# Kernel tuning notes

Measured on AMD Instinct MI355X. Metric: run time of the kernel, lower is better.

The kernel has to match this reference:

```python
import jax, jax.numpy as jnp
import numpy as np

B, C, L = 8192, 1, 4096
SCALES = 5
OUT_DIM = 512
STD_FACTOR = 1.0
SQRT_HALF = 0.7071067811865476  # Haar filter coefficient 1/sqrt(2)


def setup_inputs() -> dict:
    key = jax.random.key(0)
    k1, k2 = jax.random.split(key)
    x = jax.random.normal(k1, (B, C, L), dtype=jnp.float32)
    # kaiming_uniform_(a=0): bound = sqrt(2) * sqrt(3 / fan_in)
    fan_in = L  # in_dim_wave == in_dim for dyadic Haar
    bound = np.sqrt(2.0) * np.sqrt(3.0 / fan_in)
    block_mat = jax.random.uniform(k2, (L, OUT_DIM), dtype=jnp.float32,
                                   minval=-bound, maxval=bound)
    return {"x": x, "block_mat": block_mat}


def haar_analysis(x, scales):
    """Multi-level Haar DWT over last axis. Returns [cA_n, cD_n, ..., cD_1]."""
    details = []
    cur = x
    for _ in range(scales):
        even, odd = cur[..., ::2], cur[..., 1::2]
        details.append((even - odd) * SQRT_HALF)  # highpass
        cur = (even + odd) * SQRT_HALF            # lowpass
    return [cur] + details[::-1]


def reference(x, block_mat):
    coeffs = haar_analysis(x, SCALES)
    x_freq_cat = jnp.concatenate(coeffs, axis=-1)        # [B, C, L]
    c_no = x_freq_cat.shape[-1]
    x_freq_mat = x_freq_cat.reshape(-1, c_no)            # [B*C, L]
    a = jnp.abs(x_freq_mat)
    # torch.std is unbiased (ddof=1)
    threshold = jnp.mean(a) + jnp.std(a, ddof=1) * STD_FACTOR
    mask = a > threshold
    # sparse.mm(sparse(masked x), W) == (x * mask) @ W
    x_sparse = jnp.where(mask, x_freq_mat, jnp.zeros((), x_freq_mat.dtype))
    out = jax.nn.relu(x_sparse @ block_mat)              # [B*C, OUT_DIM]
    return out.reshape(x_freq_cat.shape[:-1] + (OUT_DIM,))
```

## Files before the change

### kernel.cpp

```cpp
#include <hip/hip_runtime.h>
#include <hip/hip_bf16.h>
#include <math.h>

#define LDIM 4096
#define NROWS 8192
#define NOUT 512

static const float SQRT_HALF_F = 0.70710678118654752440f;

typedef __attribute__((ext_vector_type(8))) short short8;
typedef __attribute__((ext_vector_type(4))) float f32x4;
typedef __attribute__((ext_vector_type(8))) unsigned short u16x8;
typedef __attribute__((ext_vector_type(4))) unsigned short u16x4;
typedef __attribute__((ext_vector_type(2))) unsigned short u16x2;

#define AM_OFF   0ull
#define WT_OFF   67108864ull
#define PART_OFF (WT_OFF + 4194304ull)
#define THR_OFF  (PART_OFF + 131072ull)

__device__ inline unsigned short f2bf(float f) {
  union { float f; unsigned u; } v; v.f = f;
  unsigned r = (v.u + 0x7fffu + ((v.u >> 16) & 1u)) >> 16;
  return (unsigned short)r;
}

__device__ inline unsigned short mcvt(float f, float thr) {
  return f2bf((fabsf(f) > thr) ? f : 0.0f);
}

__device__ inline void async16(void* l, const void* g) {
  __builtin_amdgcn_global_load_lds((const __attribute__((address_space(1))) void*)g,
                                   (__attribute__((address_space(3))) void*)l, 16, 0, 0);
}

__global__ __launch_bounds__(256) void haar1_kernel(const float* __restrict__ x,
                                                    double* __restrict__ partials,
                                                    const float* __restrict__ W,
                                                    unsigned short* __restrict__ Wt) {
  if (blockIdx.x >= NROWS) {
    __shared__ float tile[32][33];
    const int wb = blockIdx.x - NROWS;
    const int bx = wb & 15;
    const int by = wb >> 4;
    const int tx = threadIdx.x & 31, ty = threadIdx.x >> 5;
#pragma unroll
    for (int j = 0; j < 4; ++j)
      tile[ty + j * 8][tx] = W[(size_t)(by * 32 + ty + j * 8) * NOUT + bx * 32 + tx];
    __syncthreads();
#pragma unroll
    for (int j = 0; j < 4; ++j)
      Wt[(size_t)(bx * 32 + ty + j * 8) * LDIM + by * 32 + tx] = f2bf(tile[tx][ty + j * 8]);
    return;
  }

  __shared__ double red[8];
  const int row = blockIdx.x;
  const int t = threadIdx.x;
  const float S = SQRT_HALF_F;

  const float4* xr = (const float4*)(x + (size_t)row * LDIM) + 4 * t;
  float v[16];
#pragma unroll
  for (int k = 0; k < 4; ++k) {
    float4 q = xr[k];
    v[4 * k] = q.x; v[4 * k + 1] = q.y; v[4 * k + 2] = q.z; v[4 * k + 3] = q.w;
  }

  double sa = 0.0, sq = 0.0;
  float a1[8], a2[4], a3[2], a4;
#pragma unroll
  for (int j = 0; j < 8; ++j) {
    float d = (v[2 * j] - v[2 * j + 1]) * S;
    a1[j] = (v[2 * j] + v[2 * j + 1]) * S;
    sa += (double)fabsf(d); sq += (double)d * (double)d;
  }
#pragma unroll
  for (int j = 0; j < 4; ++j) {
    float d = (a1[2 * j] - a1[2 * j + 1]) * S;
    a2[j] = (a1[2 * j] + a1[2 * j + 1]) * S;
    sa += (double)fabsf(d); sq += (double)d * (double)d;
  }
#pragma unroll
  for (int j = 0; j < 2; ++j) {
    float d = (a2[2 * j] - a2[2 * j + 1]) * S;
    a3[j] = (a2[2 * j] + a2[2 * j + 1]) * S;
    sa += (double)fabsf(d); sq += (double)d * (double)d;
  }
  {
    float d = (a3[0] - a3[1]) * S;
    a4 = (a3[0] + a3[1]) * S;
    sa += (double)fabsf(d); sq += (double)d * (double)d;
  }
  {
    float other = __shfl_xor(a4, 1, 64);
    if ((t & 1) == 0) {
      float d = (a4 - other) * S, ap = (a4 + other) * S;
      sa += (double)fabsf(d) + (double)fabsf(ap);
      sq += (double)d * (double)d + (double)ap * (double)ap;
    }
  }

  const int lane = t & 63, wid = t >> 6;
#pragma unroll
  for (int off = 32; off > 0; off >>= 1) {
    sa += __shfl_down(sa, off, 64);
    sq += __shfl_down(sq, off, 64);
  }
  if (lane == 0) { red[wid] = sa; red[4 + wid] = sq; }
  __syncthreads();
  if (t == 0) {
    partials[2 * (size_t)row + 0] = red[0] + red[1] + red[2] + red[3];
    partials[2 * (size_t)row + 1] = red[4] + red[5] + red[6] + red[7];
  }
}

__global__ __launch_bounds__(1024) void thr_kernel(const double* __restrict__ partials,
                                                   float* __restrict__ thr) {
  __shared__ double red[32];
  const int tid = threadIdx.x;
  double sa = 0.0, sq = 0.0;
#pragma unroll
  for (int k = 0; k < NROWS / 1024; ++k) {
    int i = tid + k * 1024;
    sa += partials[2 * i + 0];
    sq += partials[2 * i + 1];
  }
  const int lane = tid & 63, wid = tid >> 6;
#pragma unroll
  for (int off = 32; off > 0; off >>= 1) {
    sa += __shfl_down(sa, off, 64);
    sq += __shfl_down(sq, off, 64);
  }
  if (lane == 0) { red[wid] = sa; red[16 + wid] = sq; }
  __syncthreads();
  if (tid == 0) {
    double s = 0.0, q = 0.0;
#pragma unroll
    for (int i = 0; i < 16; ++i) { s += red[i]; q += red[16 + i]; }
    const double n = (double)NROWS * (double)LDIM;
    double mean = s / n;
    double var = (q - s * s / n) / (n - 1.0);
    *thr = (float)(mean + sqrt(var));
  }
}

__global__ __launch_bounds__(256) void haar2_kernel(const float* __restrict__ x,
                                                    const float* __restrict__ thrp,
                                                    unsigned short* __restrict__ Am) {
  const float thr = *thrp;
  const int row = blockIdx.x;
  const int t = threadIdx.x;
  const float S = SQRT_HALF_F;

  const float4* xr = (const float4*)(x + (size_t)row * LDIM) + 4 * t;
  float v[16];
#pragma unroll
  for (int k = 0; k < 4; ++k) {
    float4 q = xr[k];
    v[4 * k] = q.x; v[4 * k + 1] = q.y; v[4 * k + 2] = q.z; v[4 * k + 3] = q.w;
  }

  unsigned short* orow = Am + (size_t)row * LDIM;
  float a1[8], a2[4], a3[2], a4;

  u16x8 d1;
#pragma unroll
  for (int j = 0; j < 8; ++j) {
    float d = (v[2 * j] - v[2 * j + 1]) * S;
    a1[j] = (v[2 * j] + v[2 * j + 1]) * S;
    d1[j] = mcvt(d, thr);
  }
  *(u16x8*)(orow + 2048 + 8 * t) = d1;

  u16x4 d2;
#pragma unroll
  for (int j = 0; j < 4; ++j) {
    float d = (a1[2 * j] - a1[2 * j + 1]) * S;
    a2[j] = (a1[2 * j] + a1[2 * j + 1]) * S;
    d2[j] = mcvt(d, thr);
  }
  *(u16x4*)(orow + 1024 + 4 * t) = d2;

  u16x2 d3;
#pragma unroll
  for (int j = 0; j < 2; ++j) {
    float d = (a2[2 * j] - a2[2 * j + 1]) * S;
    a3[j] = (a2[2 * j] + a2[2 * j + 1]) * S;
    d3[j] = mcvt(d, thr);
  }
  *(u16x2*)(orow + 512 + 2 * t) = d3;

  {
    float d = (a3[0] - a3[1]) * S;
    a4 = (a3[0] + a3[1]) * S;
    orow[256 + t] = mcvt(d, thr);
  }
  {
    float other = __shfl_xor(a4, 1, 64);
    if ((t & 1) == 0) {
      float d = (a4 - other) * S, ap = (a4 + other) * S;
      orow[128 + t / 2] = mcvt(d, thr);
      orow[t / 2] = mcvt(ap, thr);
    }
  }
}

__global__ __launch_bounds__(512) void gemm_kernel(const unsigned short* __restrict__ Am,
                                                   const unsigned short* __restrict__ Wt,
                                                   float* __restrict__ out) {
  __shared__ __align__(16) unsigned short As[128 * 64];
  __shared__ __align__(16) unsigned short Bs[64 * 64];

  const int tid = threadIdx.x;
  const int lane = tid & 63, w = tid >> 6;
  const int quad = lane >> 4, l15 = lane & 15;
  const int wm = w >> 1, wn = w & 1;

  const int id = blockIdx.x;
  const int xcd = id & 7, slot = id >> 3;
  const int nblk = slot & 7;
  const int mblk = (slot >> 3) * 8 + xcd;
  const int n0 = nblk * 64, m0 = mblk * 128;

  f32x4 acc[2][2] = {};

  const int rl = lane >> 3;
  const int cg = (lane & 7) ^ rl;
  const unsigned short* AgBase = Am + (size_t)(m0 + rl) * LDIM + cg * 8;
  const unsigned short* BgBase = Wt + (size_t)(n0 + rl) * LDIM + cg * 8;

  for (int k0 = 0; k0 < LDIM; k0 += 64) {
#pragma unroll
    for (int j = 0; j < 2; ++j)
      async16(&As[(w * 2 + j) * 512], AgBase + (size_t)((w * 2 + j) * 8) * LDIM + k0);
    async16(&Bs[w * 512], BgBase + (size_t)(w * 8) * LDIM + k0);
    __syncthreads();

    short8 af[2][2], bf[2][2];
#pragma unroll
    for (int mi = 0; mi < 2; ++mi) {
      const int row = wm * 32 + mi * 16 + l15;
#pragma unroll
      for (int ks = 0; ks < 2; ++ks)
        af[mi][ks] = *(const short8*)&As[row * 64 + ((ks * 4 + quad) ^ (row & 7)) * 8];
    }
#pragma unroll
    for (int ni = 0; ni < 2; ++ni) {
      const int row = wn * 32 + ni * 16 + l15;
#pragma unroll
      for (int ks = 0; ks < 2; ++ks)
        bf[ni][ks] = *(const short8*)&Bs[row * 64 + ((ks * 4 + quad) ^ (row & 7)) * 8];
    }
#pragma unroll
    for (int ks = 0; ks < 2; ++ks)
#pragma unroll
      for (int mi = 0; mi < 2; ++mi)
#pragma unroll
        for (int ni = 0; ni < 2; ++ni)
          acc[mi][ni] = __builtin_amdgcn_mfma_f32_16x16x32_bf16(af[mi][ks], bf[ni][ks],
                                                                acc[mi][ni], 0, 0, 0);
    __syncthreads();
  }

#pragma unroll
  for (int mi = 0; mi < 2; ++mi) {
#pragma unroll
    for (int ni = 0; ni < 2; ++ni) {
      const int r0 = m0 + wm * 32 + mi * 16 + quad * 4;
      const int c = n0 + wn * 32 + ni * 16 + l15;
#pragma unroll
      for (int r = 0; r < 4; ++r)
        out[(size_t)(r0 + r) * NOUT + c] = fmaxf(acc[mi][ni][r], 0.0f);
    }
  }
}

extern "C" void kernel_launch(void* const* d_in, const int* in_sizes, int n_in,
                              void* d_out, int out_size, void* d_ws, size_t ws_size,
                              hipStream_t stream) {
  const float* x = (const float*)d_in[0];
  const float* W = (const float*)d_in[1];
  float* out = (float*)d_out;

  char* ws = (char*)d_ws;
  unsigned short* Am = (unsigned short*)(ws + AM_OFF);
  unsigned short* Wt = (unsigned short*)(ws + WT_OFF);
  double* partials = (double*)(ws + PART_OFF);
  float* thr = (float*)(ws + THR_OFF);

  haar1_kernel<<<NROWS + 2048, 256, 0, stream>>>(x, partials, W, Wt);
  thr_kernel<<<1, 1024, 0, stream>>>(partials, thr);
  haar2_kernel<<<NROWS, 256, 0, stream>>>(x, thr, Am);
  gemm_kernel<<<512, 512, 0, stream>>>(Am, Wt, out);
}
```

Before: 269.0 us.

## Double-buffer GEMM shared-memory tiles to overlap async loads with MFMA compute

The GEMM main loop now uses two LDS buffers for the A and B tiles. It issues async global-to-LDS loads for the next k-tile before computing on the current one, with a single waitcnt plus barrier per iteration instead of two syncs. The aim is to hide global memory latency behind MFMA work. It doubles LDS usage, which may reduce occupancy. There is also a possible hazard: the next stage's loads target the other buffer while slower waves may still be reading it from the previous iteration, since only one barrier separates them.

```diff
diff --git a/kernel.cpp b/kernel.cpp
--- a/kernel.cpp
+++ b/kernel.cpp
@@ -206,11 +206,38 @@
   }
 }
 
+#define GEMM_COMPUTE(ASB, BSB)                                                        \
+  {                                                                                   \
+    short8 af[2][2], bf[2][2];                                                        \
+    _Pragma("unroll")                                                                 \
+    for (int mi = 0; mi < 2; ++mi) {                                                  \
+      const int arow = wm * 32 + mi * 16 + l15;                                       \
+      _Pragma("unroll")                                                               \
+      for (int ks = 0; ks < 2; ++ks)                                                  \
+        af[mi][ks] = *(const short8*)&(ASB)[arow * 64 + ((ks * 4 + quad) ^ (arow & 7)) * 8]; \
+    }                                                                                 \
+    _Pragma("unroll")                                                                 \
+    for (int ni = 0; ni < 2; ++ni) {                                                  \
+      const int brow = wn * 32 + ni * 16 + l15;                                       \
+      _Pragma("unroll")                                                               \
+      for (int ks = 0; ks < 2; ++ks)                                                  \
+        bf[ni][ks] = *(const short8*)&(BSB)[brow * 64 + ((ks * 4 + quad) ^ (brow & 7)) * 8]; \
+    }                                                                                 \
+    _Pragma("unroll")                                                                 \
+    for (int ks = 0; ks < 2; ++ks)                                                    \
+      _Pragma("unroll")                                                               \
+      for (int mi = 0; mi < 2; ++mi)                                                  \
+        _Pragma("unroll")                                                             \
+        for (int ni = 0; ni < 2; ++ni)                                                \
+          acc[mi][ni] = __builtin_amdgcn_mfma_f32_16x16x32_bf16(af[mi][ks], bf[ni][ks], \
+                                                                acc[mi][ni], 0, 0, 0); \
+  }
+
 __global__ __launch_bounds__(512) void gemm_kernel(const unsigned short* __restrict__ Am,
                                                    const unsigned short* __restrict__ Wt,
                                                    float* __restrict__ out) {
-  __shared__ __align__(16) unsigned short As[128 * 64];
-  __shared__ __align__(16) unsigned short Bs[64 * 64];
+  __shared__ __align__(16) unsigned short As[2][128 * 64];
+  __shared__ __align__(16) unsigned short Bs[2][64 * 64];
 
   const int tid = threadIdx.x;
   const int lane = tid & 63, w = tid >> 6;
@@ -230,38 +257,29 @@
   const unsigned short* AgBase = Am + (size_t)(m0 + rl) * LDIM + cg * 8;
   const unsigned short* BgBase = Wt + (size_t)(n0 + rl) * LDIM + cg * 8;
 
-  for (int k0 = 0; k0 < LDIM; k0 += 64) {
-#pragma unroll
-    for (int j = 0; j < 2; ++j)
-      async16(&As[(w * 2 + j) * 512], AgBase + (size_t)((w * 2 + j) * 8) * LDIM + k0);
-    async16(&Bs[w * 512], BgBase + (size_t)(w * 8) * LDIM + k0);
-    __syncthreads();
-
-    short8 af[2][2], bf[2][2];
-#pragma unroll
-    for (int mi = 0; mi < 2; ++mi) {
-      const int row = wm * 32 + mi * 16 + l15;
-#pragma unroll
-      for (int ks = 0; ks < 2; ++ks)
-        af[mi][ks] = *(const short8*)&As[row * 64 + ((ks * 4 + quad) ^ (row & 7)) * 8];
-    }
-#pragma unroll
-    for (int ni = 0; ni < 2; ++ni) {
-      const int row = wn * 32 + ni * 16 + l15;
-#pragma unroll
-      for (int ks = 0; ks < 2; ++ks)
-        bf[ni][ks] = *(const short8*)&Bs[row * 64 + ((ks * 4 + quad) ^ (row & 7)) * 8];
-    }
-#pragma unroll
-    for (int ks = 0; ks < 2; ++ks)
-#pragma unroll
-      for (int mi = 0; mi < 2; ++mi)
-#pragma unroll
-        for (int ni = 0; ni < 2; ++ni)
-          acc[mi][ni] = __builtin_amdgcn_mfma_f32_16x16x32_bf16(af[mi][ks], bf[ni][ks],
-                                                                acc[mi][ni], 0, 0, 0);
-    __syncthreads();
-  }
+#define GEMM_STAGE(buf, k0)                                                            \
+  {                                                                                    \
+    _Pragma("unroll")                                                                  \
+    for (int j = 0; j < 2; ++j)                                                        \
+      async16(&As[buf][(w * 2 + j) * 512], AgBase + (size_t)((w * 2 + j) * 8) * LDIM + (k0)); \
+    async16(&Bs[buf][w * 512], BgBase + (size_t)(w * 8) * LDIM + (k0));                \
+  }
+
+  GEMM_STAGE(0, 0);
+  asm volatile("s_waitcnt vmcnt(0)" ::: "memory");
+  __builtin_amdgcn_s_barrier();
+  __builtin_amdgcn_sched_barrier(0);
+
+  int cur = 0;
+  for (int t = 0; t < (LDIM / 64) - 1; ++t) {
+    GEMM_STAGE(cur ^ 1, (t + 1) * 64);
+    GEMM_COMPUTE(As[cur], Bs[cur]);
+    asm volatile("s_waitcnt vmcnt(0)" ::: "memory");
+    __builtin_amdgcn_s_barrier();
+    __builtin_amdgcn_sched_barrier(0);
+    cur ^= 1;
+  }
+  GEMM_COMPUTE(As[cur], Bs[cur]);
 
 #pragma unroll
   for (int mi = 0; mi < 2; ++mi) {
```

New measurement: 266.4 us. About the same (-1.0%).
